# Performance work log

Measured on AMD Instinct MI355X. Metric: run time of the kernel, lower is better.

The kernel has to match this reference:

```python
import jax, jax.numpy as jnp
import numpy as np

K, D, B, T = 512, 256, 32, 4096

def setup_inputs() -> dict:
    key = jax.random.key(0)
    k1, k2 = jax.random.split(key)
    z_e_x = jax.random.normal(k1, (B, D, T), dtype=jnp.float32)
    # nn.Embedding weight init uniform(-1/K, 1/K)
    emb_weight = jax.random.uniform(k2, (K, D), dtype=jnp.float32, minval=-1.0 / K, maxval=1.0 / K)
    return {"z_e_x": z_e_x, "emb_weight": emb_weight}

def reference(z_e_x, emb_weight):
    # forward(): permute [B,D,T] -> [B,T,D], nearest-codebook indices
    z = jnp.transpose(z_e_x, (0, 2, 1))  # [B, T, D]
    # squared L2 distances: ||z||^2 - 2 z.W^T + ||W||^2  -> [B, T, K]
    z_sq = jnp.sum(z * z, axis=-1, keepdims=True)           # [B, T, 1]
    w_sq = jnp.sum(emb_weight * emb_weight, axis=-1)        # [K]
    cross = jnp.einsum('btd,kd->btk', z, emb_weight)        # [B, T, K]
    dists = z_sq - 2.0 * cross + w_sq[None, None, :]
    latents = jnp.argmin(dists, axis=-1)                    # [B, T] int
    return latents
```

## Files before the change

### kernel.cpp

```cpp
#include <hip/hip_runtime.h>
#include <math.h>

#define NK 512
#define DD 256
#define NB 32
#define NT 4096

typedef __attribute__((ext_vector_type(8))) _Float16 f16x8;
typedef __attribute__((ext_vector_type(4))) float f32x4;

#define MARGIN 1.5e-4f
#define DCH 16
#define NCH 16
#define ASTR 536
#define ZCROWS 65536
#define PCAP   524288
#define PBCAP  8192

__device__ __forceinline__ unsigned short f16bits(float x) {
    _Float16 h = (_Float16)x;
    unsigned short s;
    __builtin_memcpy(&s, &h, 2);
    return s;
}

__global__ __launch_bounds__(512) void prep_kernel(const float* __restrict__ W,
                                                   unsigned short* __restrict__ Wpp,
                                                   float* __restrict__ wsq,
                                                   int* __restrict__ gcnt,
                                                   int* __restrict__ pcnt,
                                                   int* __restrict__ oflow) {
    const int bx = blockIdx.x;
    const int k  = threadIdx.x;
    if (bx < NCH) {
        const int d0 = bx * DCH;
        float w[16];
        const float4* src4 = (const float4*)(W + (size_t)k * DD + d0);
        #pragma unroll
        for (int q = 0; q < 4; ++q) {
            float4 v = src4[q];
            w[4 * q + 0] = v.x; w[4 * q + 1] = v.y; w[4 * q + 2] = v.z; w[4 * q + 3] = v.w;
        }
        __align__(16) unsigned int dw[16];
        #pragma unroll
        for (int j = 0; j < 16; ++j) {
            unsigned short s = f16bits(w[j] * 4096.0f);
            dw[j] = (unsigned int)s | ((unsigned int)s << 16);
        }
        unsigned short* dst = Wpp + ((size_t)bx * 512 + k) * 32;
        #pragma unroll
        for (int j = 0; j < 4; ++j) ((int4*)dst)[j] = ((const int4*)dw)[j];
    } else {
        const float4* row = (const float4*)(W + (size_t)k * DD);
        double s = 0.0;
        #pragma unroll 8
        for (int i = 0; i < DD / 4; ++i) {
            float4 v = row[i];
            s += (double)v.x * v.x + (double)v.y * v.y + (double)v.z * v.z + (double)v.w * v.w;
        }
        wsq[k] = (float)s;
        if (k == 0) *gcnt = 0;
        if (k == 1) *pcnt = 0;
        if (k == 2) *oflow = 0;
    }
}

__global__ __launch_bounds__(512, 4) void vq_phase1(const float* __restrict__ Z,
                                                    const unsigned short* __restrict__ Wpp,
                                                    const float* __restrict__ wsq,
                                                    int* __restrict__ out,
                                                    int* __restrict__ gties,
                                                    int* __restrict__ gcnt,
                                                    float* __restrict__ Zc,
                                                    float* __restrict__ zq,
                                                    unsigned long long* __restrict__ slots,
                                                    int* __restrict__ gpairs,
                                                    int* __restrict__ pcnt,
                                                    int* __restrict__ oflow) {
    __shared__ __align__(16) short As[64 * ASTR];
    __shared__ int lcnt, gbase, pcl, pbase_sh, pcl_sh;

    const int tid  = threadIdx.x;
    const int wave = tid >> 6;
    const int lane = tid & 63;
    const int lm   = lane & 15;
    const int lq   = lane >> 4;
    const int nw   = wave;

    const int bx = blockIdx.x;
    const int b  = bx >> 6;
    const int t0 = (bx & 63) * 64;

    const int t_l = tid & 63;
    const int dgs = (tid >> 6) & 3;

    if (tid == 0) { lcnt = 0; pcl = 0; }

    double zacc = 0.0;
    if (tid < 256) {
        const float* zcol = Z + (size_t)b * DD * NT + t0 + t_l;
        #pragma unroll
        for (int g = 0; g < 8; ++g) {
            float zv[8];
            #pragma unroll
            for (int j = 0; j < 8; ++j)
                zv[j] = zcol[(size_t)(dgs * 64 + g * 8 + j) * NT];
            #pragma unroll
            for (int j = 0; j < 8; ++j)
                zacc = fma((double)zv[j], (double)zv[j], zacc);
            __align__(16) unsigned int u[8];
            #pragma unroll
            for (int j = 0; j < 8; ++j) {
                float z = zv[j];
                _Float16 zh = (_Float16)z;
                float rz = z - (float)zh;
                unsigned short hs, ls;
                __builtin_memcpy(&hs, &zh, 2);
                ls = f16bits(rz);
                u[j] = (unsigned int)hs | ((unsigned int)ls << 16);
            }
            int4* dst = (int4*)&As[t_l * ASTR + dgs * 128 + g * 16];
            dst[0] = ((const int4*)u)[0];
            dst[1] = ((const int4*)u)[1];
        }
    }

    const unsigned short* wb = Wpp + ((size_t)(nw * 64 + lm) * 32) + lq * 8;
    int4 bv0[4], bv1[4];
    #pragma unroll
    for (int nt = 0; nt < 4; ++nt)
        bv0[nt] = *(const int4*)(wb + nt * 512);

    __syncthreads();

    f32x4 acc[4][4];
    #pragma unroll
    for (int mt = 0; mt < 4; ++mt)
        #pragma unroll
        for (int nt = 0; nt < 4; ++nt)
            acc[mt][nt] = (f32x4){0.f, 0.f, 0.f, 0.f};

    #pragma unroll
    for (int c = 0; c < NCH; ++c) {
        int4* cur = (c & 1) ? bv1 : bv0;
        int4* nxt = (c & 1) ? bv0 : bv1;
        if (c < NCH - 1) {
            const unsigned short* wp = wb + (size_t)(c + 1) * 16384;
            #pragma unroll
            for (int nt = 0; nt < 4; ++nt)
                nxt[nt] = *(const int4*)(wp + nt * 512);
        }
        f16x8 a[4];
        #pragma unroll
        for (int mt = 0; mt < 4; ++mt)
            a[mt] = *(const f16x8*)&As[(mt * 16 + lm) * ASTR + c * 32 + lq * 8];
        #pragma unroll
        for (int mt = 0; mt < 4; ++mt)
            #pragma unroll
            for (int nt = 0; nt < 4; ++nt)
                acc[mt][nt] = __builtin_amdgcn_mfma_f32_16x16x32_f16(
                    a[mt], *(const f16x8*)&cur[nt], acc[mt][nt], 0, 0, 0);
    }

    __syncthreads();
    char* base = (char*)As;
    double* zred  = (double*)base;
    float*  zf    = (float*)(base + 2048);
    float*  qf    = (float*)(base + 2304);
    int*    tia   = (int*)(base + 2560);
    int*    ltok  = (int*)(base + 2816);
    float*  col   = (float*)(base + 3072);
    double* pzz   = (double*)(base + 4096);
    float*  cb1   = (float*)(base + 4608);
    float*  cb2   = (float*)(base + 6656);
    int*    cbi   = (int*)(base + 8704);
    int*    plist = (int*)(base + 10752);

    if (tid < 256) zred[dgs * 64 + t_l] = zacc;
    __syncthreads();
    if (tid < 64) {
        double s = zred[tid];
        #pragma unroll
        for (int p = 1; p < 4; ++p) s += zred[p * 64 + tid];
        zf[tid] = (float)s;
    }
    __syncthreads();

    float wq[4];
    #pragma unroll
    for (int nt = 0; nt < 4; ++nt)
        wq[nt] = wsq[nw * 64 + nt * 16 + lm];
    const int kbase = nw * 64 + lm;

    #pragma unroll
    for (int mt = 0; mt < 4; ++mt) {
        #pragma unroll
        for (int r = 0; r < 4; ++r) {
            float zz = zf[mt * 16 + lq * 4 + r];
            float q1 = INFINITY, q2 = INFINITY;
            int i1 = 0x7fffffff;
            #pragma unroll
            for (int nt = 0; nt < 4; ++nt) {
                float c2   = __fmul_rn(acc[mt][nt][r], 4.8828125e-4f);
                float dist = __fadd_rn(__fsub_rn(zz, c2), wq[nt]);
                int kk = kbase + nt * 16;
                if (dist < q1 || (dist == q1 && kk < i1)) { q2 = q1; q1 = dist; i1 = kk; }
                else if (dist < q2) q2 = dist;
            }
            #pragma unroll
            for (int mk = 1; mk <= 8; mk <<= 1) {
                float o1 = __shfl_xor(q1, mk);
                float o2 = __shfl_xor(q2, mk);
                int   oi = __shfl_xor(i1, mk);
                if (o1 < q1 || (o1 == q1 && oi < i1)) { q2 = fminf(q1, o2); q1 = o1; i1 = oi; }
                else { q2 = fminf(o1, q2); }
            }
            if (lm == 0) {
                int m = mt * 16 + lq * 4 + r;
                cb1[m * 8 + nw] = q1;
                cb2[m * 8 + nw] = q2;
                cbi[m * 8 + nw] = i1;
            }
        }
    }
    __syncthreads();
    if (tid < 64) {
        float q1 = cb1[tid * 8], q2 = cb2[tid * 8];
        int   i1 = cbi[tid * 8];
        #pragma unroll
        for (int p = 1; p < 8; ++p) {
            float c1 = cb1[tid * 8 + p], c2v = cb2[tid * 8 + p];
            int   ci = cbi[tid * 8 + p];
            if (c1 < q1 || (c1 == q1 && ci < i1)) { q2 = fminf(q1, c2v); q1 = c1; i1 = ci; }
            else { q2 = fminf(q2, c1); }
        }
        out[(size_t)b * NT + t0 + tid] = i1;
        qf[tid] = q1;
        int ta = -1;
        if (q2 - q1 <= MARGIN) {
            ta = atomicAdd(&lcnt, 1);
            ltok[ta] = tid;
        }
        tia[tid] = ta;
    }
    __syncthreads();
    if (tid == 0) gbase = (lcnt > 0) ? atomicAdd(gcnt, lcnt) : 0;
    __syncthreads();

    const int nloc = lcnt;
    for (int i = 0; i < nloc; ++i) {
        const int tok = ltok[i];
        const int ti  = gbase + i;
        if (ti < ZCROWS) {
            if (tid < 256) {
                float v = Z[(size_t)b * DD * NT + (size_t)tid * NT + (t0 + tok)];
                Zc[(size_t)ti * 256 + tid] = v;
                col[tid] = v;
            }
        } else if (tid == 0) {
            *oflow = 1;
        }
        if (tid == 0) {
            gties[ti] = b * NT + t0 + tok;
            slots[ti] = 0xFFFFFFFFFFFFFFFFULL;
        }
        __syncthreads();
        if (ti < ZCROWS) {
            if (tid < 32) {
                double s = 0.0;
                #pragma unroll
                for (int j = 0; j < 8; ++j) {
                    double zz = (double)col[tid * 8 + j];
                    s = fma(zz, zz, s);
                }
                pzz[tid] = s;
            }
        }
        __syncthreads();
        if (ti < ZCROWS && tid == 0) {
            double s = 0.0;
            #pragma unroll
            for (int j = 0; j < 32; ++j) s += pzz[j];
            zq[ti] = (float)s;
        }
        __syncthreads();
    }

    if (nloc > 0) {
        #pragma unroll
        for (int mt = 0; mt < 4; ++mt) {
            #pragma unroll
            for (int r = 0; r < 4; ++r) {
                const int tok = mt * 16 + lq * 4 + r;
                const int ta  = tia[tok];
                if (ta < 0) continue;
                const int ti = gbase + ta;
                if (ti >= ZCROWS) continue;
                const float thr = qf[tok] + MARGIN;
                const float zz  = zf[tok];
                #pragma unroll
                for (int nt = 0; nt < 4; ++nt) {
                    float c2   = __fmul_rn(acc[mt][nt][r], 4.8828125e-4f);
                    float dist = __fadd_rn(__fsub_rn(zz, c2), wq[nt]);
                    if (dist <= thr) {
                        int p = atomicAdd(&pcl, 1);
                        if (p < PBCAP) plist[p] = (ti << 9) | (kbase + nt * 16);
                    }
                }
            }
        }
    }
    __syncthreads();
    if (tid == 0) {
        int take = pcl;
        int bs = (take > 0) ? atomicAdd(pcnt, take) : 0;
        pbase_sh = bs;
        pcl_sh = take;
        if (take > PBCAP || bs + take > PCAP) *oflow = 1;
    }
    __syncthreads();
    {
        int take = pcl_sh; if (take > PBCAP) take = PBCAP;
        for (int j = tid; j < take; j += 512) {
            int gp = pbase_sh + j;
            if (gp < PCAP) gpairs[gp] = plist[j];
        }
    }
}

__global__ __launch_bounds__(256) void vq_fix_pairs(const float* __restrict__ W,
                                                    const float* __restrict__ wsq,
                                                    const float* __restrict__ Zc,
                                                    const float* __restrict__ zq,
                                                    const int* __restrict__ gpairs,
                                                    const int* __restrict__ pcnt,
                                                    unsigned long long* __restrict__ slots) {
    int np = *pcnt;
    if (np > PCAP) np = PCAP;
    for (int j = blockIdx.x * 256 + threadIdx.x; j < np; j += (int)gridDim.x * 256) {
        const int p  = gpairs[j];
        const int ti = p >> 9;
        const int k  = p & 511;
        const float4* zr = (const float4*)(Zc + (size_t)ti * 256);
        const float4* wr = (const float4*)(W + (size_t)k * DD);
        float a8 = 0.f;
        #pragma unroll 4
        for (int q = 0; q < 64; ++q) {
            float4 w4 = wr[q];
            float4 z4 = zr[q];
            a8 = fmaf(z4.x, w4.x, a8);
            a8 = fmaf(z4.y, w4.y, a8);
            a8 = fmaf(z4.z, w4.z, a8);
            a8 = fmaf(z4.w, w4.w, a8);
        }
        float da = __fadd_rn(__fsub_rn(zq[ti], __fmul_rn(2.0f, a8)), wsq[k]);
        unsigned long long key =
            ((unsigned long long)__float_as_uint(da) << 32) | (unsigned int)k;
        atomicMin(&slots[ti], key);
    }
}

__global__ __launch_bounds__(256) void vq_final(const int* __restrict__ gties,
                                                const int* __restrict__ gcnt,
                                                const int* __restrict__ oflow,
                                                const unsigned long long* __restrict__ slots,
                                                int* __restrict__ out) {
    if (*oflow) return;
    const int n = *gcnt;
    for (int j = blockIdx.x * 256 + threadIdx.x; j < n; j += (int)gridDim.x * 256) {
        out[gties[j]] = (int)(slots[j] & 511ULL);
    }
}

__global__ __launch_bounds__(256) void vq_fix(const float* __restrict__ Z,
                                              const float* __restrict__ W,
                                              const float* __restrict__ wsq,
                                              const int* __restrict__ gties,
                                              const int* __restrict__ gcnt,
                                              int* __restrict__ out,
                                              const int* __restrict__ oflow) {
    if (oflow != nullptr && *oflow == 0) return;

    __shared__ __align__(16) float Zs[8][256];
    __shared__ double pz[8][32];
    __shared__ float  zsqs[8];
    __shared__ int    bts[8];
    __shared__ float  rv[8][4];
    __shared__ int    ri[8][4];

    const int tid  = threadIdx.x;
    const int lane = tid & 63;
    const int wvx  = tid >> 6;
    const int n    = *gcnt;

    for (int base = blockIdx.x * 8; base < n; base += (int)gridDim.x * 8) {
        const int m = (n - base < 8) ? (n - base) : 8;
        __syncthreads();
        if (tid < 8) bts[tid] = gties[base + ((tid < m) ? tid : 0)];
        __syncthreads();

        #pragma unroll
        for (int i = 0; i < 8; ++i) {
            if (i < m) {
                int tb = bts[i];
                int bb = tb >> 12, t = tb & 4095;
                Zs[i][tid] = Z[(size_t)bb * DD * NT + (size_t)tid * NT + t];
            }
        }
        __syncthreads();

        {
            int i = tid >> 5, seg = tid & 31;
            double s = 0.0;
            #pragma unroll
            for (int j = 0; j < 8; ++j) {
                double zz = (double)Zs[i][seg * 8 + j];
                s = fma(zz, zz, s);
            }
            pz[i][seg] = s;
        }
        __syncthreads();
        if (tid < 8) {
            double s = 0.0;
            #pragma unroll
            for (int j = 0; j < 32; ++j) s += pz[tid][j];
            zsqs[tid] = (float)s;
        }
        __syncthreads();

        float da[2][8];
        #pragma unroll
        for (int rr = 0; rr < 2; ++rr) {
            int k = tid + rr * 256;
            const float4* wr = (const float4*)(W + (size_t)k * DD);
            float a8[8];
            #pragma unroll
            for (int i = 0; i < 8; ++i) a8[i] = 0.f;
            #pragma unroll 2
            for (int q = 0; q < 64; ++q) {
                float4 w4 = wr[q];
                #pragma unroll
                for (int i = 0; i < 8; ++i) {
                    float4 z4 = *(const float4*)&Zs[i][4 * q];
                    a8[i] = fmaf(z4.x, w4.x, a8[i]);
                    a8[i] = fmaf(z4.y, w4.y, a8[i]);
                    a8[i] = fmaf(z4.z, w4.z, a8[i]);
                    a8[i] = fmaf(z4.w, w4.w, a8[i]);
                }
            }
            float wqv = wsq[k];
            #pragma unroll
            for (int i = 0; i < 8; ++i)
                da[rr][i] = __fadd_rn(__fsub_rn(zsqs[i], __fmul_rn(2.0f, a8[i])), wqv);
        }

        #pragma unroll
        for (int i = 0; i < 8; ++i) {
            float v = da[0][i]; int ix = tid;
            if (da[1][i] < v) { v = da[1][i]; ix = tid + 256; }
            #pragma unroll
            for (int mk = 1; mk <= 32; mk <<= 1) {
                float ov = __shfl_xor(v, mk);
                int   oi = __shfl_xor(ix, mk);
                if (ov < v || (ov == v && oi < ix)) { v = ov; ix = oi; }
            }
            if (lane == 0) { rv[i][wvx] = v; ri[i][wvx] = ix; }
        }
        __syncthreads();
        if (tid < 8 && tid < m) {
            float v = INFINITY; int ix = 0x7fffffff;
            #pragma unroll
            for (int w = 0; w < 4; ++w) {
                if (rv[tid][w] < v || (rv[tid][w] == v && ri[tid][w] < ix)) {
                    v = rv[tid][w]; ix = ri[tid][w];
                }
            }
            out[bts[tid]] = ix;
        }
    }
}

__global__ __launch_bounds__(256, 2) void vq_phase1_reg(const float* __restrict__ Z,
                                                        const unsigned short* __restrict__ Wpp,
                                                        const float* __restrict__ wsq,
                                                        int* __restrict__ out,
                                                        int* __restrict__ gties,
                                                        int* __restrict__ gcnt) {
    __shared__ __align__(16) short As[64 * ASTR];
    __shared__ int lcnt, gbase;

    const int tid  = threadIdx.x;
    const int wave = tid >> 6;
    const int lane = tid & 63;
    const int lm   = lane & 15;
    const int lq   = lane >> 4;
    const int nw   = wave;

    const int bx = blockIdx.x;
    const int b  = bx >> 6;
    const int t0 = (bx & 63) * 64;

    const int t_l = tid & 63;
    const int dgs = tid >> 6;

    const float* zcol = Z + (size_t)b * DD * NT + t0 + t_l;

    if (tid == 0) lcnt = 0;

    double zacc = 0.0;
    #pragma unroll
    for (int half = 0; half < 2; ++half) {
        float zv[32];
        #pragma unroll
        for (int j = 0; j < 32; ++j)
            zv[j] = zcol[(size_t)(dgs * 64 + half * 32 + j) * NT];
        #pragma unroll
        for (int j = 0; j < 32; ++j)
            zacc = fma((double)zv[j], (double)zv[j], zacc);
        #pragma unroll
        for (int j0 = 0; j0 < 32; j0 += 4) {
            __align__(16) unsigned int u[4];
            #pragma unroll
            for (int q = 0; q < 4; ++q) {
                float z = zv[j0 + q];
                _Float16 zh = (_Float16)z;
                float rz = z - (float)zh;
                unsigned short hs, ls;
                __builtin_memcpy(&hs, &zh, 2);
                ls = f16bits(rz);
                u[q] = (unsigned int)hs | ((unsigned int)ls << 16);
            }
            *(int4*)&As[t_l * ASTR + (dgs * 64 + half * 32 + j0) * 2] = *(const int4*)u;
        }
    }
    __syncthreads();

    const unsigned short* wb = Wpp + ((size_t)(nw * 128 + lm) * 32) + lq * 8;

    f32x4 acc[4][8];
    #pragma unroll
    for (int mt = 0; mt < 4; ++mt)
        #pragma unroll
        for (int nt = 0; nt < 8; ++nt)
            acc[mt][nt] = (f32x4){0.f, 0.f, 0.f, 0.f};

    int4 bv0[8], bv1[8];
    #pragma unroll
    for (int nt = 0; nt < 8; ++nt)
        bv0[nt] = *(const int4*)(wb + nt * 512);

    #pragma unroll
    for (int c = 0; c < NCH; ++c) {
        int4* cur = (c & 1) ? bv1 : bv0;
        int4* nxt = (c & 1) ? bv0 : bv1;
        if (c < NCH - 1) {
            const unsigned short* wp = wb + (size_t)(c + 1) * 16384;
            #pragma unroll
            for (int nt = 0; nt < 8; ++nt)
                nxt[nt] = *(const int4*)(wp + nt * 512);
        }
        f16x8 a[4];
        #pragma unroll
        for (int mt = 0; mt < 4; ++mt)
            a[mt] = *(const f16x8*)&As[(mt * 16 + lm) * ASTR + c * 32 + lq * 8];
        #pragma unroll
        for (int mt = 0; mt < 4; ++mt)
            #pragma unroll
            for (int nt = 0; nt < 8; ++nt)
                acc[mt][nt] = __builtin_amdgcn_mfma_f32_16x16x32_f16(
                    a[mt], *(const f16x8*)&cur[nt], acc[mt][nt], 0, 0, 0);
    }

    __syncthreads();
    double* zred = (double*)As;
    float*  zf   = (float*)(As + 1024);
    float*  cb1  = (float*)(As + 1536);
    float*  cb2  = (float*)(As + 2048);
    int*    cbi  = (int*)(As + 2560);
    int*    llist = (int*)(As + 3072);

    zred[dgs * 64 + t_l] = zacc;
    __syncthreads();
    if (tid < 64) {
        double s = zred[tid];
        #pragma unroll
        for (int p = 1; p < 4; ++p) s += zred[p * 64 + tid];
        zf[tid] = (float)s;
    }
    __syncthreads();

    float wq[8];
    #pragma unroll
    for (int nt = 0; nt < 8; ++nt)
        wq[nt] = wsq[nw * 128 + nt * 16 + lm];
    const int kbase = nw * 128 + lm;

    #pragma unroll
    for (int mt = 0; mt < 4; ++mt) {
        #pragma unroll
        for (int r = 0; r < 4; ++r) {
            float zz = zf[mt * 16 + lq * 4 + r];
            float q1 = INFINITY, q2 = INFINITY;
            int i1 = 0x7fffffff;
            #pragma unroll
            for (int nt = 0; nt < 8; ++nt) {
                float c2   = __fmul_rn(acc[mt][nt][r], 4.8828125e-4f);
                float dist = __fadd_rn(__fsub_rn(zz, c2), wq[nt]);
                int kk = kbase + nt * 16;
                if (dist < q1 || (dist == q1 && kk < i1)) { q2 = q1; q1 = dist; i1 = kk; }
                else if (dist < q2) q2 = dist;
            }
            #pragma unroll
            for (int mk = 1; mk <= 8; mk <<= 1) {
                float o1 = __shfl_xor(q1, mk);
                float o2 = __shfl_xor(q2, mk);
                int   oi = __shfl_xor(i1, mk);
                if (o1 < q1 || (o1 == q1 && oi < i1)) { q2 = fminf(q1, o2); q1 = o1; i1 = oi; }
                else { q2 = fminf(o1, q2); }
            }
            if (lm == 0) {
                int m = mt * 16 + lq * 4 + r;
                cb1[m * 4 + nw] = q1;
                cb2[m * 4 + nw] = q2;
                cbi[m * 4 + nw] = i1;
            }
        }
    }
    __syncthreads();
    if (tid < 64) {
        float q1 = cb1[tid * 4], q2 = cb2[tid * 4];
        int   i1 = cbi[tid * 4];
        #pragma unroll
        for (int p = 1; p < 4; ++p) {
            float c1 = cb1[tid * 4 + p], c2v = cb2[tid * 4 + p];
            int   ci = cbi[tid * 4 + p];
            if (c1 < q1 || (c1 == q1 && ci < i1)) { q2 = fminf(q1, c2v); q1 = c1; i1 = ci; }
            else { q2 = fminf(q2, c1); }
        }
        out[(size_t)b * NT + t0 + tid] = i1;
        if (q2 - q1 <= MARGIN) {
            int p = atomicAdd(&lcnt, 1);
            llist[p] = b * NT + t0 + tid;
        }
    }
    __syncthreads();
    if (tid == 0) gbase = (lcnt > 0) ? atomicAdd(gcnt, lcnt) : 0;
    __syncthreads();
    if (tid < lcnt) gties[gbase + tid] = llist[tid];
}

#define BT 128
#define BK 128
#define DCHUNK 32
#define NKC (NK / BK)
#define NDC (DD / DCHUNK)
#define WSTR (BK + 4)

__global__ __launch_bounds__(256) void vq_fallback(const float* __restrict__ Z,
                                                   const float* __restrict__ W,
                                                   int* __restrict__ out) {
    __shared__ __align__(16) float Zs[DCHUNK * BT];
    __shared__ __align__(16) float Ws[DCHUNK * WSTR];
    __shared__ float wsqs[NK];

    const int tid = threadIdx.x;
    const int tx  = tid & 15;
    const int ty  = tid >> 4;
    const int b   = blockIdx.y;
    const int t0  = blockIdx.x * BT;

    for (int k = tid; k < NK; k += 256) {
        const float4* row = (const float4*)(W + (size_t)k * DD);
        double s = 0.0;
        for (int i = 0; i < DD / 4; ++i) {
            float4 v = row[i];
            s += (double)v.x * v.x + (double)v.y * v.y + (double)v.z * v.z + (double)v.w * v.w;
        }
        wsqs[k] = (float)s;
    }

    const float* Zb = Z + (size_t)b * DD * NT + t0;

    float best[8]; int bidx[8];
    #pragma unroll
    for (int a = 0; a < 8; ++a) { best[a] = INFINITY; bidx[a] = 0x7fffffff; }
    double zsqd[8];
    #pragma unroll
    for (int a = 0; a < 8; ++a) zsqd[a] = 0.0;
    float zsqf[8];

    for (int kc = 0; kc < NKC; ++kc) {
        float acc[8][8];
        #pragma unroll
        for (int a = 0; a < 8; ++a)
            #pragma unroll
            for (int c = 0; c < 8; ++c) acc[a][c] = 0.f;

        for (int dc = 0; dc < NDC; ++dc) {
            const int d0 = dc * DCHUNK;
            __syncthreads();
            #pragma unroll
            for (int i = 0; i < 4; ++i) {
                int f  = tid + i * 256;
                int r  = f >> 5;
                int c4 = f & 31;
                float4 v = *(const float4*)(Zb + (size_t)(d0 + r) * NT + c4 * 4);
                *(float4*)(&Zs[r * BT + c4 * 4]) = v;
            }
            #pragma unroll
            for (int i = 0; i < 4; ++i) {
                int u  = tid + i * 256;
                int k  = u >> 3;
                int rg = u & 7;
                float4 v = *(const float4*)(W + (size_t)(kc * BK + k) * DD + d0 + rg * 4);
                Ws[(rg * 4 + 0) * WSTR + k] = v.x;
                Ws[(rg * 4 + 1) * WSTR + k] = v.y;
                Ws[(rg * 4 + 2) * WSTR + k] = v.z;
                Ws[(rg * 4 + 3) * WSTR + k] = v.w;
            }
            __syncthreads();
            #pragma unroll 4
            for (int d = 0; d < DCHUNK; ++d) {
                float4 z0 = *(const float4*)(&Zs[d * BT + ty * 8]);
                float4 z1 = *(const float4*)(&Zs[d * BT + ty * 8 + 4]);
                float4 w0 = *(const float4*)(&Ws[d * WSTR + tx * 8]);
                float4 w1 = *(const float4*)(&Ws[d * WSTR + tx * 8 + 4]);
                float za[8] = {z0.x, z0.y, z0.z, z0.w, z1.x, z1.y, z1.z, z1.w};
                float wa[8] = {w0.x, w0.y, w0.z, w0.w, w1.x, w1.y, w1.z, w1.w};
                if (kc == 0) {
                    #pragma unroll
                    for (int a = 0; a < 8; ++a)
                        zsqd[a] = fma((double)za[a], (double)za[a], zsqd[a]);
                }
                #pragma unroll
                for (int a = 0; a < 8; ++a)
                    #pragma unroll
                    for (int c = 0; c < 8; ++c)
                        acc[a][c] = fmaf(za[a], wa[c], acc[a][c]);
            }
        }
        if (kc == 0) {
            #pragma unroll
            for (int a = 0; a < 8; ++a) zsqf[a] = (float)zsqd[a];
        }
        #pragma unroll
        for (int c = 0; c < 8; ++c) {
            int   kg = kc * BK + tx * 8 + c;
            float wqv = wsqs[kg];
            #pragma unroll
            for (int a = 0; a < 8; ++a) {
                float c2   = __fmul_rn(2.0f, acc[a][c]);
                float s    = __fsub_rn(zsqf[a], c2);
                float dist = __fadd_rn(s, wqv);
                if (dist < best[a] || (dist == best[a] && kg < bidx[a])) {
                    best[a] = dist; bidx[a] = kg;
                }
            }
        }
    }
    __syncthreads();
    float* redv = Zs;
    int*   redi = (int*)Ws;
    #pragma unroll
    for (int a = 0; a < 8; ++a) {
        int tl2 = ty * 8 + a;
        redv[tl2 * 16 + tx] = best[a];
        redi[tl2 * 16 + tx] = bidx[a];
    }
    __syncthreads();
    if (tid < BT) {
        float bv = INFINITY; int bi = 0x7fffffff;
        #pragma unroll
        for (int j = 0; j < 16; ++j) {
            float v = redv[tid * 16 + j];
            int   i = redi[tid * 16 + j];
            if (v < bv || (v == bv && i < bi)) { bv = v; bi = i; }
        }
        out[(size_t)b * NT + t0 + tid] = bi;
    }
}

extern "C" void kernel_launch(void* const* d_in, const int* in_sizes, int n_in,
                              void* d_out, int out_size, void* d_ws, size_t ws_size,
                              hipStream_t stream) {
    const float* Z = (const float*)d_in[0];
    const float* W = (const float*)d_in[1];
    int* out = (int*)d_out;

    const size_t OFF_WSQ  = 0;
    const size_t OFF_CNT  = 2048;
    const size_t OFF_PCNT = 2052;
    const size_t OFF_OFL  = 2056;
    const size_t OFF_ZQ   = 4096;
    const size_t OFF_WPP  = OFF_ZQ + 524288;
    const size_t OFF_TIE  = OFF_WPP + 524288;
    const size_t OFF_SLOT = OFF_TIE + 524288;
    const size_t OFF_PAIR = OFF_SLOT + 1048576;
    const size_t OFF_ZC   = OFF_PAIR + (size_t)PCAP * 4;
    const size_t NEED_BIG = OFF_ZC + (size_t)ZCROWS * 1024;

    const size_t T2_WSQ = 0;
    const size_t T2_CNT = 2048;
    const size_t T2_WPP = 4096;
    const size_t T2_TIE = T2_WPP + 524288;
    const size_t NEED_T2 = T2_TIE + 524288;

    if (ws_size >= NEED_BIG) {
        float* wsq  = (float*)((char*)d_ws + OFF_WSQ);
        int*   gcnt = (int*)((char*)d_ws + OFF_CNT);
        int*   pcnt = (int*)((char*)d_ws + OFF_PCNT);
        int*   ofl  = (int*)((char*)d_ws + OFF_OFL);
        float* zq   = (float*)((char*)d_ws + OFF_ZQ);
        unsigned short* wpp = (unsigned short*)((char*)d_ws + OFF_WPP);
        int*   gties = (int*)((char*)d_ws + OFF_TIE);
        unsigned long long* slots = (unsigned long long*)((char*)d_ws + OFF_SLOT);
        int*   gpairs = (int*)((char*)d_ws + OFF_PAIR);
        float* zc   = (float*)((char*)d_ws + OFF_ZC);

        prep_kernel<<<dim3(NCH + 1), dim3(512), 0, stream>>>(W, wpp, wsq, gcnt, pcnt, ofl);
        vq_phase1<<<dim3(2048), dim3(512), 0, stream>>>(Z, wpp, wsq, out, gties, gcnt,
                                                        zc, zq, slots, gpairs, pcnt, ofl);
        vq_fix_pairs<<<dim3(512), dim3(256), 0, stream>>>(W, wsq, zc, zq, gpairs, pcnt, slots);
        vq_fix<<<dim3(256), dim3(256), 0, stream>>>(Z, W, wsq, gties, gcnt, out, ofl);
        vq_final<<<dim3(256), dim3(256), 0, stream>>>(gties, gcnt, ofl, slots, out);
    } else if (ws_size >= NEED_T2) {
        float* wsq  = (float*)((char*)d_ws + T2_WSQ);
        int*   gcnt = (int*)((char*)d_ws + T2_CNT);
        unsigned short* wpp = (unsigned short*)((char*)d_ws + T2_WPP);
        int*   gties = (int*)((char*)d_ws + T2_TIE);

        prep_kernel<<<dim3(NCH + 1), dim3(512), 0, stream>>>(W, wpp, wsq, gcnt, gcnt, gcnt);
        vq_phase1_reg<<<dim3(2048), dim3(256), 0, stream>>>(Z, wpp, wsq, out, gties, gcnt);
        vq_fix<<<dim3(256), dim3(256), 0, stream>>>(Z, W, wsq, gties, gcnt, out, nullptr);
    } else {
        vq_fallback<<<dim3(NT / BT, NB), dim3(256), 0, stream>>>(Z, W, out);
    }
}
```

Before: 337.9 us.

## Batch tie-token gathering and emit pair candidates via count-then-write

Replaces the per-tie-token serial loop, which needed three block barriers per token, with one batched gather of all tied tokens' columns into shared memory, plus a per-thread norm computation. Candidate pairs are now counted per thread first and then written directly to global memory after one global atomic reservation, so the shared-memory pair list and its cap are gone. It also raises wave priority around the MFMA block. The cost is recomputing the distance test twice, a full 64x256 strided gather loop even when only a few tokens tie, and a changed overflow path: when the block exceeds ZCROWS it now skips all Zc writes rather than only the rows past the limit.

```diff
diff --git a/kernel.cpp b/kernel.cpp
--- a/kernel.cpp
+++ b/kernel.cpp
@@ -15,7 +15,6 @@
 #define ASTR 536
 #define ZCROWS 65536
 #define PCAP   524288
-#define PBCAP  8192
 
 __device__ __forceinline__ unsigned short f16bits(float x) {
     _Float16 h = (_Float16)x;
@@ -78,7 +77,7 @@
                                                     int* __restrict__ pcnt,
                                                     int* __restrict__ oflow) {
     __shared__ __align__(16) short As[64 * ASTR];
-    __shared__ int lcnt, gbase, pcl, pbase_sh, pcl_sh;
+    __shared__ int lcnt, gbase, pcl, pcl2, pbase_sh;
 
     const int tid  = threadIdx.x;
     const int wave = tid >> 6;
@@ -94,7 +93,7 @@
     const int t_l = tid & 63;
     const int dgs = (tid >> 6) & 3;
 
-    if (tid == 0) { lcnt = 0; pcl = 0; }
+    if (tid == 0) { lcnt = 0; pcl = 0; pcl2 = 0; }
 
     double zacc = 0.0;
     if (tid < 256) {
@@ -154,12 +153,14 @@
         #pragma unroll
         for (int mt = 0; mt < 4; ++mt)
             a[mt] = *(const f16x8*)&As[(mt * 16 + lm) * ASTR + c * 32 + lq * 8];
+        __builtin_amdgcn_s_setprio(1);
         #pragma unroll
         for (int mt = 0; mt < 4; ++mt)
             #pragma unroll
             for (int nt = 0; nt < 4; ++nt)
                 acc[mt][nt] = __builtin_amdgcn_mfma_f32_16x16x32_f16(
                     a[mt], *(const f16x8*)&cur[nt], acc[mt][nt], 0, 0, 0);
+        __builtin_amdgcn_s_setprio(0);
     }
 
     __syncthreads();
@@ -169,12 +170,10 @@
     float*  qf    = (float*)(base + 2304);
     int*    tia   = (int*)(base + 2560);
     int*    ltok  = (int*)(base + 2816);
-    float*  col   = (float*)(base + 3072);
-    double* pzz   = (double*)(base + 4096);
-    float*  cb1   = (float*)(base + 4608);
-    float*  cb2   = (float*)(base + 6656);
-    int*    cbi   = (int*)(base + 8704);
-    int*    plist = (int*)(base + 10752);
+    float*  cb1   = (float*)(base + 3072);
+    float*  cb2   = (float*)(base + 5120);
+    int*    cbi   = (int*)(base + 7168);
+    float*  colbuf = (float*)(base + 3072);
 
     if (tid < 256) zred[dgs * 64 + t_l] = zacc;
     __syncthreads();
@@ -248,45 +247,42 @@
     __syncthreads();
 
     const int nloc = lcnt;
-    for (int i = 0; i < nloc; ++i) {
-        const int tok = ltok[i];
-        const int ti  = gbase + i;
-        if (ti < ZCROWS) {
-            if (tid < 256) {
-                float v = Z[(size_t)b * DD * NT + (size_t)tid * NT + (t0 + tok)];
-                Zc[(size_t)ti * 256 + tid] = v;
-                col[tid] = v;
-            }
-        } else if (tid == 0) {
-            *oflow = 1;
-        }
-        if (tid == 0) {
-            gties[ti] = b * NT + t0 + tok;
-            slots[ti] = 0xFFFFFFFFFFFFFFFFULL;
+    if (nloc == 0) return;
+
+    const bool ofl_loc = (gbase + nloc > ZCROWS);
+    if (ofl_loc && tid == 0) *oflow = 1;
+
+    if (tid < nloc) gties[gbase + tid] = b * NT + t0 + ltok[tid];
+
+    if (!ofl_loc) {
+        if (tid < nloc) slots[gbase + tid] = 0xFFFFFFFFFFFFFFFFULL;
+        for (int j = tid; j < 64 * 256; j += 512) {
+            const int d = j >> 6;
+            const int i = j & 63;
+            const int ic = (i < nloc) ? i : (nloc - 1);
+            const float v = Z[(size_t)b * DD * NT + (size_t)d * NT + (t0 + ltok[ic])];
+            if (i < nloc) {
+                colbuf[i * 256 + d] = v;
+                Zc[(size_t)(gbase + i) * 256 + d] = v;
+            }
         }
         __syncthreads();
-        if (ti < ZCROWS) {
-            if (tid < 32) {
+        if (tid < nloc) {
+            const float* cp = colbuf + tid * 256;
+            double tot = 0.0;
+            for (int seg = 0; seg < 32; ++seg) {
                 double s = 0.0;
                 #pragma unroll
-                for (int j = 0; j < 8; ++j) {
-                    double zz = (double)col[tid * 8 + j];
+                for (int jj = 0; jj < 8; ++jj) {
+                    double zz = (double)cp[seg * 8 + jj];
                     s = fma(zz, zz, s);
                 }
-                pzz[tid] = s;
-            }
-        }
-        __syncthreads();
-        if (ti < ZCROWS && tid == 0) {
-            double s = 0.0;
-            #pragma unroll
-            for (int j = 0; j < 32; ++j) s += pzz[j];
-            zq[ti] = (float)s;
-        }
-        __syncthreads();
-    }
-
-    if (nloc > 0) {
+                tot += s;
+            }
+            zq[gbase + tid] = (float)tot;
+        }
+
+        int myc = 0;
         #pragma unroll
         for (int mt = 0; mt < 4; ++mt) {
             #pragma unroll
@@ -294,36 +290,48 @@
                 const int tok = mt * 16 + lq * 4 + r;
                 const int ta  = tia[tok];
                 if (ta < 0) continue;
-                const int ti = gbase + ta;
-                if (ti >= ZCROWS) continue;
                 const float thr = qf[tok] + MARGIN;
                 const float zz  = zf[tok];
                 #pragma unroll
                 for (int nt = 0; nt < 4; ++nt) {
                     float c2   = __fmul_rn(acc[mt][nt][r], 4.8828125e-4f);
                     float dist = __fadd_rn(__fsub_rn(zz, c2), wq[nt]);
-                    if (dist <= thr) {
-                        int p = atomicAdd(&pcl, 1);
-                        if (p < PBCAP) plist[p] = (ti << 9) | (kbase + nt * 16);
+                    if (dist <= thr) ++myc;
+                }
+            }
+        }
+        if (myc) atomicAdd(&pcl, myc);
+        __syncthreads();
+        if (tid == 0) {
+            int take = pcl;
+            int bs = (take > 0) ? atomicAdd(pcnt, take) : 0;
+            pbase_sh = bs;
+            if (bs + take > PCAP) *oflow = 1;
+        }
+        __syncthreads();
+        if (myc) {
+            #pragma unroll
+            for (int mt = 0; mt < 4; ++mt) {
+                #pragma unroll
+                for (int r = 0; r < 4; ++r) {
+                    const int tok = mt * 16 + lq * 4 + r;
+                    const int ta  = tia[tok];
+                    if (ta < 0) continue;
+                    const int ti = gbase + ta;
+                    const float thr = qf[tok] + MARGIN;
+                    const float zz  = zf[tok];
+                    #pragma unroll
+                    for (int nt = 0; nt < 4; ++nt) {
+                        float c2   = __fmul_rn(acc[mt][nt][r], 4.8828125e-4f);
+                        float dist = __fadd_rn(__fsub_rn(zz, c2), wq[nt]);
+                        if (dist <= thr) {
+                            int p = atomicAdd(&pcl2, 1);
+                            int gp = pbase_sh + p;
+                            if (gp < PCAP) gpairs[gp] = (ti << 9) | (kbase + nt * 16);
+                        }
                     }
                 }
             }
-        }
-    }
-    __syncthreads();
-    if (tid == 0) {
-        int take = pcl;
-        int bs = (take > 0) ? atomicAdd(pcnt, take) : 0;
-        pbase_sh = bs;
-        pcl_sh = take;
-        if (take > PBCAP || bs + take > PCAP) *oflow = 1;
-    }
-    __syncthreads();
-    {
-        int take = pcl_sh; if (take > PBCAP) take = PBCAP;
-        for (int j = tid; j < take; j += 512) {
-            int gp = pbase_sh + j;
-            if (gp < PCAP) gpairs[gp] = plist[j];
         }
     }
 }
```

Measured after the change: 367.8 us. 1.09x slower.

## Drop per-token column staging in phase1; gather Z directly in pair fixup

Applied to the files above, without the earlier changes.

Phase1 no longer copies each near-tie token's 256-element Z column into a compact buffer, and no longer computes its squared norm in a serialized per-token loop with three block barriers per token. Blocks with no ties now exit early, and tie bookkeeping is written in parallel. The pair-fix kernel instead gathers the column straight from Z with strided loads and recomputes ||z||^2 itself for every pair. This trades the phase1 serialization and the staging traffic for uncoalesced strided reads and redundant norm work in the fixup. The removed ZCROWS cap also drops an overflow guard, and the fixup grid is halved.

```diff
diff --git a/kernel.cpp b/kernel.cpp
--- a/kernel.cpp
+++ b/kernel.cpp
@@ -13,9 +13,8 @@
 #define DCH 16
 #define NCH 16
 #define ASTR 536
-#define ZCROWS 65536
 #define PCAP   524288
-#define PBCAP  8192
+#define PBCAP  4096
 
 __device__ __forceinline__ unsigned short f16bits(float x) {
     _Float16 h = (_Float16)x;
@@ -71,14 +70,12 @@
                                                     int* __restrict__ out,
                                                     int* __restrict__ gties,
                                                     int* __restrict__ gcnt,
-                                                    float* __restrict__ Zc,
-                                                    float* __restrict__ zq,
                                                     unsigned long long* __restrict__ slots,
                                                     int* __restrict__ gpairs,
                                                     int* __restrict__ pcnt,
                                                     int* __restrict__ oflow) {
     __shared__ __align__(16) short As[64 * ASTR];
-    __shared__ int lcnt, gbase, pcl, pbase_sh, pcl_sh;
+    __shared__ int lcnt, gbase, pcl, pbase_sh;
 
     const int tid  = threadIdx.x;
     const int wave = tid >> 6;
@@ -169,12 +166,10 @@
     float*  qf    = (float*)(base + 2304);
     int*    tia   = (int*)(base + 2560);
     int*    ltok  = (int*)(base + 2816);
-    float*  col   = (float*)(base + 3072);
-    double* pzz   = (double*)(base + 4096);
-    float*  cb1   = (float*)(base + 4608);
-    float*  cb2   = (float*)(base + 6656);
-    int*    cbi   = (int*)(base + 8704);
-    int*    plist = (int*)(base + 10752);
+    float*  cb1   = (float*)(base + 3072);
+    float*  cb2   = (float*)(base + 5120);
+    int*    cbi   = (int*)(base + 7168);
+    int*    plist = (int*)(base + 9216);
 
     if (tid < 256) zred[dgs * 64 + t_l] = zacc;
     __syncthreads();
@@ -244,68 +239,34 @@
         tia[tid] = ta;
     }
     __syncthreads();
-    if (tid == 0) gbase = (lcnt > 0) ? atomicAdd(gcnt, lcnt) : 0;
-    __syncthreads();
-
     const int nloc = lcnt;
-    for (int i = 0; i < nloc; ++i) {
-        const int tok = ltok[i];
-        const int ti  = gbase + i;
-        if (ti < ZCROWS) {
-            if (tid < 256) {
-                float v = Z[(size_t)b * DD * NT + (size_t)tid * NT + (t0 + tok)];
-                Zc[(size_t)ti * 256 + tid] = v;
-                col[tid] = v;
-            }
-        } else if (tid == 0) {
-            *oflow = 1;
-        }
-        if (tid == 0) {
-            gties[ti] = b * NT + t0 + tok;
-            slots[ti] = 0xFFFFFFFFFFFFFFFFULL;
-        }
-        __syncthreads();
-        if (ti < ZCROWS) {
-            if (tid < 32) {
-                double s = 0.0;
-                #pragma unroll
-                for (int j = 0; j < 8; ++j) {
-                    double zz = (double)col[tid * 8 + j];
-                    s = fma(zz, zz, s);
-                }
-                pzz[tid] = s;
-            }
-        }
-        __syncthreads();
-        if (ti < ZCROWS && tid == 0) {
-            double s = 0.0;
-            #pragma unroll
-            for (int j = 0; j < 32; ++j) s += pzz[j];
-            zq[ti] = (float)s;
-        }
-        __syncthreads();
-    }
-
-    if (nloc > 0) {
-        #pragma unroll
-        for (int mt = 0; mt < 4; ++mt) {
-            #pragma unroll
-            for (int r = 0; r < 4; ++r) {
-                const int tok = mt * 16 + lq * 4 + r;
-                const int ta  = tia[tok];
-                if (ta < 0) continue;
-                const int ti = gbase + ta;
-                if (ti >= ZCROWS) continue;
-                const float thr = qf[tok] + MARGIN;
-                const float zz  = zf[tok];
-                #pragma unroll
-                for (int nt = 0; nt < 4; ++nt) {
-                    float c2   = __fmul_rn(acc[mt][nt][r], 4.8828125e-4f);
-                    float dist = __fadd_rn(__fsub_rn(zz, c2), wq[nt]);
-                    if (dist <= thr) {
-                        int p = atomicAdd(&pcl, 1);
-                        if (p < PBCAP) plist[p] = (ti << 9) | (kbase + nt * 16);
-                    }
+    if (nloc == 0) return;
+
+    if (tid == 0) gbase = atomicAdd(gcnt, nloc);
+    __syncthreads();
+
+    if (tid < nloc) {
+        gties[gbase + tid] = b * NT + t0 + ltok[tid];
+        slots[gbase + tid] = 0xFFFFFFFFFFFFFFFFULL;
+    }
+
+    #pragma unroll
+    for (int mt = 0; mt < 4; ++mt) {
+        #pragma unroll
+        for (int r = 0; r < 4; ++r) {
+            const int tok = mt * 16 + lq * 4 + r;
+            const int ta  = tia[tok];
+            if (ta < 0) continue;
+            const int ti  = gbase + ta;
+            const float thr = qf[tok] + MARGIN;
+            const float zz  = zf[tok];
+            #pragma unroll
+            for (int nt = 0; nt < 4; ++nt) {
+                float c2   = __fmul_rn(acc[mt][nt][r], 4.8828125e-4f);
+                float dist = __fadd_rn(__fsub_rn(zz, c2), wq[nt]);
+                if (dist <= thr) {
+                    int p = atomicAdd(&pcl, 1);
+                    if (p < PBCAP) plist[p] = (ti << 9) | (kbase + nt * 16);
                 }
             }
         }
@@ -313,14 +274,13 @@
     __syncthreads();
     if (tid == 0) {
         int take = pcl;
-        int bs = (take > 0) ? atomicAdd(pcnt, take) : 0;
+        int bs = atomicAdd(pcnt, take);
         pbase_sh = bs;
-        pcl_sh = take;
         if (take > PBCAP || bs + take > PCAP) *oflow = 1;
     }
     __syncthreads();
     {
-        int take = pcl_sh; if (take > PBCAP) take = PBCAP;
+        int take = pcl; if (take > PBCAP) take = PBCAP;
         for (int j = tid; j < take; j += 512) {
             int gp = pbase_sh + j;
             if (gp < PCAP) gpairs[gp] = plist[j];
@@ -328,10 +288,10 @@
     }
 }
 
-__global__ __launch_bounds__(256) void vq_fix_pairs(const float* __restrict__ W,
+__global__ __launch_bounds__(256) void vq_fix_pairs(const float* __restrict__ Z,
+                                                    const float* __restrict__ W,
                                                     const float* __restrict__ wsq,
-                                                    const float* __restrict__ Zc,
-                                                    const float* __restrict__ zq,
+                                                    const int* __restrict__ gties,
                                                     const int* __restrict__ gpairs,
                                                     const int* __restrict__ pcnt,
                                                     unsigned long long* __restrict__ slots) {
@@ -341,19 +301,38 @@
         const int p  = gpairs[j];
         const int ti = p >> 9;
         const int k  = p & 511;
-        const float4* zr = (const float4*)(Zc + (size_t)ti * 256);
+        const int bt = gties[ti];
+        const int bb = bt >> 12, t = bt & 4095;
+        const float* zc = Z + (size_t)bb * DD * NT + t;
         const float4* wr = (const float4*)(W + (size_t)k * DD);
+
+        double tot = 0.0;
         float a8 = 0.f;
-        #pragma unroll 4
-        for (int q = 0; q < 64; ++q) {
-            float4 w4 = wr[q];
-            float4 z4 = zr[q];
-            a8 = fmaf(z4.x, w4.x, a8);
-            a8 = fmaf(z4.y, w4.y, a8);
-            a8 = fmaf(z4.z, w4.z, a8);
-            a8 = fmaf(z4.w, w4.w, a8);
-        }
-        float da = __fadd_rn(__fsub_rn(zq[ti], __fmul_rn(2.0f, a8)), wsq[k]);
+        for (int seg = 0; seg < 32; ++seg) {
+            float zv[8];
+            #pragma unroll
+            for (int jj = 0; jj < 8; ++jj)
+                zv[jj] = zc[(size_t)(seg * 8 + jj) * NT];
+            float4 w4a = wr[seg * 2];
+            float4 w4b = wr[seg * 2 + 1];
+            double s = 0.0;
+            #pragma unroll
+            for (int jj = 0; jj < 8; ++jj) {
+                double zz = (double)zv[jj];
+                s = fma(zz, zz, s);
+            }
+            tot += s;
+            a8 = fmaf(zv[0], w4a.x, a8);
+            a8 = fmaf(zv[1], w4a.y, a8);
+            a8 = fmaf(zv[2], w4a.z, a8);
+            a8 = fmaf(zv[3], w4a.w, a8);
+            a8 = fmaf(zv[4], w4b.x, a8);
+            a8 = fmaf(zv[5], w4b.y, a8);
+            a8 = fmaf(zv[6], w4b.z, a8);
+            a8 = fmaf(zv[7], w4b.w, a8);
+        }
+        float zqv = (float)tot;
+        float da = __fadd_rn(__fsub_rn(zqv, __fmul_rn(2.0f, a8)), wsq[k]);
         unsigned long long key =
             ((unsigned long long)__float_as_uint(da) << 32) | (unsigned int)k;
         atomicMin(&slots[ti], key);
@@ -791,13 +770,11 @@
     const size_t OFF_CNT  = 2048;
     const size_t OFF_PCNT = 2052;
     const size_t OFF_OFL  = 2056;
-    const size_t OFF_ZQ   = 4096;
-    const size_t OFF_WPP  = OFF_ZQ + 524288;
+    const size_t OFF_WPP  = 4096;
     const size_t OFF_TIE  = OFF_WPP + 524288;
     const size_t OFF_SLOT = OFF_TIE + 524288;
     const size_t OFF_PAIR = OFF_SLOT + 1048576;
-    const size_t OFF_ZC   = OFF_PAIR + (size_t)PCAP * 4;
-    const size_t NEED_BIG = OFF_ZC + (size_t)ZCROWS * 1024;
+    const size_t NEED_BIG = OFF_PAIR + (size_t)PCAP * 4;
 
     const size_t T2_WSQ = 0;
     const size_t T2_CNT = 2048;
@@ -810,17 +787,15 @@
         int*   gcnt = (int*)((char*)d_ws + OFF_CNT);
         int*   pcnt = (int*)((char*)d_ws + OFF_PCNT);
         int*   ofl  = (int*)((char*)d_ws + OFF_OFL);
-        float* zq   = (float*)((char*)d_ws + OFF_ZQ);
         unsigned short* wpp = (unsigned short*)((char*)d_ws + OFF_WPP);
         int*   gties = (int*)((char*)d_ws + OFF_TIE);
         unsigned long long* slots = (unsigned long long*)((char*)d_ws + OFF_SLOT);
         int*   gpairs = (int*)((char*)d_ws + OFF_PAIR);
-        float* zc   = (float*)((char*)d_ws + OFF_ZC);
 
         prep_kernel<<<dim3(NCH + 1), dim3(512), 0, stream>>>(W, wpp, wsq, gcnt, pcnt, ofl);
         vq_phase1<<<dim3(2048), dim3(512), 0, stream>>>(Z, wpp, wsq, out, gties, gcnt,
-                                                        zc, zq, slots, gpairs, pcnt, ofl);
-        vq_fix_pairs<<<dim3(512), dim3(256), 0, stream>>>(W, wsq, zc, zq, gpairs, pcnt, slots);
+                                                        slots, gpairs, pcnt, ofl);
+        vq_fix_pairs<<<dim3(256), dim3(256), 0, stream>>>(Z, W, wsq, gties, gpairs, pcnt, slots);
         vq_fix<<<dim3(256), dim3(256), 0, stream>>>(Z, W, wsq, gties, gcnt, out, ofl);
         vq_final<<<dim3(256), dim3(256), 0, stream>>>(gties, gcnt, ofl, slots, out);
     } else if (ws_size >= NEED_T2) {
```

After: 361.6 us. 1.07x slower.
